# Performance work log

Hardware: AMD Instinct MI355X
Metric: run time of the kernel (lower is better)

Reference implementation:

```python
import jax, jax.numpy as jnp
import numpy as np

J0 = 3
JBIG = 7
TH = 0.01
MM = 3.2 ** 2  # Gaussian window variance factor from get_phi


def get_phi(x):
    # phi(x) = sinc-like sin(pi x)/(pi x) * exp(-x^2/(2*mm)), with phi(0)=1
    t = jnp.pi * x
    t_safe = jnp.where(t == 0.0, 1.0, t)
    out = jnp.sin(t) * jnp.exp(-jnp.square(x) / (2.0 * MM)) / t_safe
    return jnp.where(t == 0.0, 1.0, out)


def nearest_idx(x, targets):
    # x: [N,1], targets: [K] -> index of nearest sample for each target, [K]
    return jnp.argmin(jnp.abs(x - targets[None, :]), axis=0)


def _outer_recon(wc, wr, C):
    # sum_{c,r} wc[:,c] wr[:,r] C[c,r]  (equivalent to the blockwise einsum +
    # tensordot over flattened (c,r) pairs in the torch code)
    return jnp.einsum('nc,cr,mr->nm', wc, C, wr)


def setup_inputs() -> dict:
    key = jax.random.key(0)
    k_img, k_xc, k_xr = jax.random.split(key, 3)
    N = 4096
    img = jax.random.normal(k_img, (N, N), dtype=jnp.float32)
    # sorted sample coordinates in [-1, 1] (domain spanned by wavelet translates)
    xc = jnp.sort(2.0 * jax.random.uniform(k_xc, (N, 1), dtype=jnp.float32) - 1.0, axis=0)
    xr = jnp.sort(2.0 * jax.random.uniform(k_xr, (N, 1), dtype=jnp.float32) - 1.0, axis=0)
    return {"img": img, "xc": xc, "xr": xr}


def reference(img, xc, xr):
    # ---- coarse approximation at scale j0 ----
    j0 = J0
    k = jnp.asarray(np.arange(-2 ** j0, 2 ** j0 + 1, 1), dtype=jnp.float32)  # [K0]
    phi_c = get_phi((2.0 ** j0) * xc - k[None, :])  # [N, K0]
    phi_r = get_phi((2.0 ** j0) * xr - k[None, :])  # [N, K0]
    xjk = k * (2.0 ** (-j0))
    ic = nearest_idx(xc, xjk)
    ir = nearest_idx(xr, xjk)
    F = img[ic[:, None], ir[None, :]]               # [K0, K0]
    approx = _outer_recon(phi_c, phi_r, F)          # [N, N]

    # ---- detail scales j0 .. J-1 ----
    for j in range(J0, JBIG):
        kj = jnp.asarray(np.arange((-2 ** (j + 1) - 1) / 2, 2 ** (j + 1) / 2, 0.5),
                         dtype=jnp.float32)          # [Kj] = 2^{j+2}+1
        xjk = (2.0 * kj + 1.0) * (2.0 ** (-j - 1))
        ic = nearest_idx(xc, xjk)
        ir = nearest_idx(xr, xjk)
        f = img[ic[:, None], ir[None, :]]            # [Kj, Kj]
        u = approx[ic[:, None], ir[None, :]]         # [Kj, Kj]
        diff = f - u
        # thresholded coefficient selection (torch.where -> mask, same math)
        D = jnp.where(jnp.abs(diff) > TH, diff, 0.0)
        psi_c = get_phi((2.0 ** (j + 1)) * xc - (2.0 * kj + 1.0)[None, :])  # [N, Kj]
        psi_r = get_phi((2.0 ** (j + 1)) * xr - (2.0 * kj + 1.0)[None, :])  # [N, Kj]
        approx = approx + _outer_recon(psi_c, psi_r, D)
    return approx
```

## Files before the change

### kernel.cpp

```cpp
#include <hip/hip_runtime.h>
#include <hip/hip_bf16.h>
#include <cstddef>
#include <cstdint>

#define NN 4096
#define KP 512
#define KTOT 501

typedef __attribute__((ext_vector_type(8))) short short8;
typedef __attribute__((ext_vector_type(4))) float f32x4;

#define GLB(p) ((const __attribute__((address_space(1))) void*)(p))
#define LDS(p) ((__attribute__((address_space(3))) void*)(p))

__device__ __forceinline__ float bf2f(unsigned short u) {
    union { unsigned int i; float f; } v; v.i = ((unsigned int)u) << 16; return v.f;
}

__device__ __forceinline__ void split_bf16(float v, unsigned short& h, unsigned short& l) {
    __hip_bfloat16 hb = __float2bfloat16(v);
    __hip_bfloat16 lb = __float2bfloat16(v - __bfloat162float(hb));
    h = *(unsigned short*)&hb;
    l = *(unsigned short*)&lb;
}

__device__ __forceinline__ float phi_eval(float x) {
    if (x == 0.0f) return 1.0f;
    const float PI_F = 3.14159265358979323846f;
    float rn = rintf(x);
    float r  = x - rn;
    float s  = __sinf(PI_F * r);
    if (((int)rn) & 1) s = -s;
    float e  = __expf(-x * x * (1.0f / 20.48f));
    return __fdividef(s * e, PI_F * x);
}

__device__ __forceinline__ void col_to_level(int col, int& l, int& off) {
    if      (col < 17)  { l = 0; off = 0;   }
    else if (col < 50)  { l = 1; off = 17;  }
    else if (col < 115) { l = 2; off = 50;  }
    else                { l = (col < 244) ? 3 : 4; off = (col < 244) ? 115 : 244; }
}

__global__ __launch_bounds__(256) void fused_pre(const float* __restrict__ xc,
                                                 const float* __restrict__ xr,
                                                 unsigned short* __restrict__ PCh,
                                                 unsigned short* __restrict__ PCl,
                                                 unsigned short* __restrict__ PRh,
                                                 unsigned short* __restrict__ PRl,
                                                 unsigned short* __restrict__ Ch,
                                                 int* __restrict__ idxAll) {
    __shared__ float sv[256];
    __shared__ int   si[256];
    const int b = blockIdx.x;
    const int tid = threadIdx.x;
    if (b < 2 * KTOT) {
        int side = (b >= KTOT);
        int col  = side ? b - KTOT : b;
        const float* x = side ? xr : xc;
        int l, off; col_to_level(col, l, off);
        int s = 8 << l;
        float target = (float)(col - off - s) / (float)s;
        float best = 1e30f; int bidx = 0;
        for (int n = tid; n < NN; n += 256) {
            float d = fabsf(x[n] - target);
            if (d < best) { best = d; bidx = n; }
        }
        sv[tid] = best; si[tid] = bidx;
        __syncthreads();
        for (int w = 128; w > 0; w >>= 1) {
            if (tid < w) {
                float ov = sv[tid + w]; int oi = si[tid + w];
                if (ov < sv[tid] || (ov == sv[tid] && oi < si[tid])) { sv[tid] = ov; si[tid] = oi; }
            }
            __syncthreads();
        }
        if (tid == 0) idxAll[b] = si[0];
    } else if (b < 2026) {
        const int i0 = (b - 1002) * 2048 + tid;
        #pragma unroll
        for (int j = 0; j < 8; ++j) {
            int i = i0 + j * 256;
            int n = i >> 9, col = i & 511;
            float pc = 0.f, pr = 0.f;
            if (col < KTOT) {
                int l, off; col_to_level(col, l, off);
                int s = 8 << l;
                float fo = (float)(col - off - s);
                float fs = (float)s;
                pc = phi_eval(fs * xc[n] - fo);
                pr = phi_eval(fs * xr[n] - fo);
            }
            unsigned short h, l2;
            split_bf16(pc, h, l2); PCh[i] = h; PCl[i] = l2;
            split_bf16(pr, h, l2); PRh[i] = h; PRl[i] = l2;
        }
    } else {
        uint4* z = (uint4*)Ch;
        const int g0 = (b - 2026) * 256 + tid;
        #pragma unroll
        for (int j = 0; j < 8; ++j) {
            int g = g0 + j * 8192;
            z[g] = make_uint4(0u, 0u, 0u, 0u);
        }
    }
}


template<int T, int OFF>
__global__ __launch_bounds__(256) void build_k(const float* __restrict__ img,
                                               const int* __restrict__ idxAll,
                                               const float* __restrict__ Usm,
                                               const unsigned short* __restrict__ PRh,
                                               const unsigned short* __restrict__ PRl,
                                               float* __restrict__ CdT,
                                               unsigned short* __restrict__ Ch,
                                               unsigned short* __restrict__ Cl) {
    int i = blockIdx.x * 256 + threadIdx.x;
    if (i >= T * T) return;
    int p = i / T, q = i - p * T;
    int ip = idxAll[OFF + p];
    int iq = idxAll[KTOT + OFF + q];
    float f = img[(size_t)ip * NN + iq];
    float val;
    if (OFF == 0) {
        val = f;
    } else {
        const float* u = Usm + (size_t)(OFF + p) * KP;
        const unsigned short* ph = PRh + (size_t)iq * KP;
        const unsigned short* pl = PRl + (size_t)iq * KP;
        float s0 = 0.f, s1 = 0.f, s2 = 0.f, s3 = 0.f;
        int k = 0;
        #pragma unroll 4
        for (; k + 4 <= OFF; k += 4) {
            ushort4 h4 = *(const ushort4*)(ph + k);
            ushort4 l4 = *(const ushort4*)(pl + k);
            float4  b4 = *(const float4*)(u + k);
            s0 += (bf2f(h4.x) + bf2f(l4.x)) * b4.x;
            s1 += (bf2f(h4.y) + bf2f(l4.y)) * b4.y;
            s2 += (bf2f(h4.z) + bf2f(l4.z)) * b4.z;
            s3 += (bf2f(h4.w) + bf2f(l4.w)) * b4.w;
        }
        float uu = (s0 + s1) + (s2 + s3);
        for (; k < OFF; ++k) uu += (bf2f(ph[k]) + bf2f(pl[k])) * u[k];
        float d = f - uu;
        val = (fabsf(d) > 0.01f) ? d : 0.0f;
    }
    size_t o = (size_t)(OFF + q) * KP + (OFF + p);
    CdT[o] = val;
    unsigned short h, l;
    split_bf16(val, h, l);
    Ch[o] = h; Cl[o] = l;
}

template<int T, int OFF>
__global__ __launch_bounds__(256) void update_k(const unsigned short* __restrict__ PCh,
                                                const unsigned short* __restrict__ PCl,
                                                const int* __restrict__ idxAll,
                                                const float* __restrict__ CdT,
                                                float* __restrict__ Usm) {
    int i = blockIdx.x * 256 + threadIdx.x;
    if (i >= KTOT * T) return;
    int r = i / T, t = i - r * T;
    const unsigned short* ah = PCh + (size_t)idxAll[r] * KP + OFF;
    const unsigned short* al = PCl + (size_t)idxAll[r] * KP + OFF;
    const float* b = CdT + (size_t)(OFF + t) * KP + OFF;
    constexpr int HEAD = (4 - (OFF & 3)) & 3;
    float s = 0.f;
    int k = 0;
    #pragma unroll
    for (; k < HEAD; ++k) s += (bf2f(ah[k]) + bf2f(al[k])) * b[k];
    float s0 = 0.f, s1 = 0.f, s2 = 0.f, s3 = 0.f;
    #pragma unroll 4
    for (; k + 4 <= T; k += 4) {
        ushort4 h4 = *(const ushort4*)(ah + k);
        ushort4 l4 = *(const ushort4*)(al + k);
        float4  b4 = *(const float4*)(b + k);
        s0 += (bf2f(h4.x) + bf2f(l4.x)) * b4.x;
        s1 += (bf2f(h4.y) + bf2f(l4.y)) * b4.y;
        s2 += (bf2f(h4.z) + bf2f(l4.z)) * b4.z;
        s3 += (bf2f(h4.w) + bf2f(l4.w)) * b4.w;
    }
    s += (s0 + s1) + (s2 + s3);
    for (; k < T; ++k) s += (bf2f(ah[k]) + bf2f(al[k])) * b[k];
    Usm[(size_t)r * KP + OFF + t] = s;
}

#define GEMM_BODY(Ahi_, Alo_, Bhi_, Blo_, XARR_, XBASE_, BMASK_)                       \
    __shared__ short As_h[2][128][32];                                                 \
    __shared__ short As_l[2][128][32];                                                 \
    __shared__ short Bs_h[2][128][32];                                                 \
    __shared__ short Bs_l[2][128][32];                                                 \
    const int tid  = threadIdx.x;                                                      \
    const int lane = tid & 63;                                                         \
    const int wave = tid >> 6;                                                         \
    const int wr   = wave >> 1;                                                        \
    const int wc   = wave & 1;                                                         \
    const int row0 = blockIdx.y * 128;                                                 \
    const int col0 = blockIdx.x * 128;                                                 \
    int list[16]; int nch = 0;                                                         \
    {                                                                                  \
        float xmn = XARR_[XBASE_];                                                     \
        float xmx = XARR_[(XBASE_) + 127];                                             \
        int mask = 0;                                                                  \
        const int off_[5] = {0, 17, 50, 115, 244};                                     \
        _Pragma("unroll")                                                              \
        for (int l = 0; l < 5; ++l) {                                                  \
            int s_ = 8 << l;                                                           \
            int clo = off_[l] + s_ + (int)floorf(s_ * xmn - 12.5f);                    \
            int chi = off_[l] + s_ + (int)ceilf (s_ * xmx + 12.5f);                    \
            if (clo < off_[l]) clo = off_[l];                                          \
            if (chi > off_[l] + 2 * s_) chi = off_[l] + 2 * s_;                        \
            for (int c = clo >> 5; c <= (chi >> 5); ++c) mask |= 1 << c;               \
        }                                                                              \
        mask &= (BMASK_);                                                              \
        for (int c = 0; c < 16; ++c) if ((mask >> c) & 1) list[nch++] = c;             \
    }                                                                                  \
    f32x4 acc[4][4];                                                                   \
    _Pragma("unroll")                                                                  \
    for (int i = 0; i < 4; ++i)                                                        \
        _Pragma("unroll")                                                              \
        for (int j = 0; j < 4; ++j) acc[i][j] = (f32x4){0.f, 0.f, 0.f, 0.f};           \
    const int srow = lane >> 2;                                                        \
    const int scol = ((lane & 3) ^ ((lane >> 3) & 3)) * 8;    \
    auto stage_ = [&](int bb, int k0) {                                                \
        _Pragma("unroll")                                                              \
        for (int s = 0; s < 2; ++s) {                                                  \
            const int rseg = wave * 32 + s * 16;                                       \
            const size_t ga = (size_t)(row0 + rseg + srow) * KP + k0 + scol;           \
            const size_t gb = (size_t)(col0 + rseg + srow) * KP + k0 + scol;           \
            __builtin_amdgcn_global_load_lds(GLB(Ahi_ + ga), LDS(&As_h[bb][rseg][0]), 16, 0, 0); \
            __builtin_amdgcn_global_load_lds(GLB(Alo_ + ga), LDS(&As_l[bb][rseg][0]), 16, 0, 0); \
            __builtin_amdgcn_global_load_lds(GLB(Bhi_ + gb), LDS(&Bs_h[bb][rseg][0]), 16, 0, 0); \
            __builtin_amdgcn_global_load_lds(GLB(Blo_ + gb), LDS(&Bs_l[bb][rseg][0]), 16, 0, 0); \
        }                                                                              \
    };                                                                                 \
    const int kbsw = 8 * ((lane >> 4) ^ ((lane >> 1) & 3));    \
    if (nch > 0) stage_(0, list[0] * 32);                                              \
    __syncthreads();                                                                   \
    for (int ic = 0; ic < nch; ++ic) {                                                 \
        const int cb = ic & 1;                                                         \
        if (ic + 1 < nch) stage_(cb ^ 1, list[ic + 1] * 32);                           \
        short8 ah[4], al[4], bh[4], bl[4];                                             \
        _Pragma("unroll")                                                              \
        for (int mb = 0; mb < 4; ++mb) {                                               \
            const int rr = wr * 64 + mb * 16 + (lane & 15);                            \
            ah[mb] = *(const short8*)&As_h[cb][rr][kbsw];                              \
            al[mb] = *(const short8*)&As_l[cb][rr][kbsw];                              \
        }                                                                              \
        _Pragma("unroll")                                                              \
        for (int nb = 0; nb < 4; ++nb) {                                               \
            const int cc = wc * 64 + nb * 16 + (lane & 15);                            \
            bh[nb] = *(const short8*)&Bs_h[cb][cc][kbsw];                              \
            bl[nb] = *(const short8*)&Bs_l[cb][cc][kbsw];                              \
        }                                                                              \
        _Pragma("unroll")                                                              \
        for (int mb = 0; mb < 4; ++mb)                                                 \
            _Pragma("unroll")                                                          \
            for (int nb = 0; nb < 4; ++nb) {                                           \
                acc[mb][nb] = __builtin_amdgcn_mfma_f32_16x16x32_bf16(ah[mb], bh[nb], acc[mb][nb], 0, 0, 0); \
                acc[mb][nb] = __builtin_amdgcn_mfma_f32_16x16x32_bf16(ah[mb], bl[nb], acc[mb][nb], 0, 0, 0); \
                acc[mb][nb] = __builtin_amdgcn_mfma_f32_16x16x32_bf16(al[mb], bh[nb], acc[mb][nb], 0, 0, 0); \
            }                                                                          \
        __syncthreads();                                                               \
    }                                                                                  \
    const int orow = (lane >> 4) * 4;                                                  \
    const int ocol = lane & 15;

__global__ __launch_bounds__(256) void gemm_mfma_f32out(const short* __restrict__ Ahi,
                                                        const short* __restrict__ Alo,
                                                        const short* __restrict__ Bhi,
                                                        const short* __restrict__ Blo,
                                                        const float* __restrict__ xr,
                                                        float* __restrict__ out) {
    GEMM_BODY(Ahi, Alo, Bhi, Blo, xr, blockIdx.x * 128, 0xFFFF)
    #pragma unroll
    for (int mb = 0; mb < 4; ++mb)
        #pragma unroll
        for (int nb = 0; nb < 4; ++nb) {
            const int col = col0 + wc * 64 + nb * 16 + ocol;
            #pragma unroll
            for (int reg = 0; reg < 4; ++reg) {
                const int row = row0 + wr * 64 + mb * 16 + orow + reg;
                out[(size_t)row * NN + col] = acc[mb][nb][reg];
            }
        }
}

__global__ __launch_bounds__(256) void gemm_mfma_splitout(const short* __restrict__ Ahi,
                                                          const short* __restrict__ Alo,
                                                          const short* __restrict__ Bhi,
                                                          const short* __restrict__ Blo,
                                                          const float* __restrict__ xc,
                                                          unsigned short* __restrict__ Oh,
                                                          unsigned short* __restrict__ Ol) {
    const int bmask_tab[4] = {0x00FF, 0xFFF8, 0xFF80, 0xFF80};
    const int bm = bmask_tab[blockIdx.x];
    GEMM_BODY(Ahi, Alo, Bhi, Blo, xc, blockIdx.y * 128, bm)
    #pragma unroll
    for (int mb = 0; mb < 4; ++mb)
        #pragma unroll
        for (int nb = 0; nb < 4; ++nb) {
            const int col = col0 + wc * 64 + nb * 16 + ocol;
            #pragma unroll
            for (int reg = 0; reg < 4; ++reg) {
                const int row = row0 + wr * 64 + mb * 16 + orow + reg;
                unsigned short h, l;
                split_bf16(acc[mb][nb][reg], h, l);
                Oh[(size_t)row * KP + col] = h;
                Ol[(size_t)row * KP + col] = l;
            }
        }
}

extern "C" void kernel_launch(void* const* d_in, const int* in_sizes, int n_in,
                              void* d_out, int out_size, void* d_ws, size_t ws_size,
                              hipStream_t stream) {
    const float* img = (const float*)d_in[0];
    const float* xc  = (const float*)d_in[1];
    const float* xr  = (const float*)d_in[2];
    float* out = (float*)d_out;

    const size_t M2 = (size_t)NN * KP;
    unsigned short* PCh = (unsigned short*)d_ws;
    unsigned short* PCl = PCh + M2;
    unsigned short* PRh = PCl + M2;
    unsigned short* PRl = PRh + M2;
    unsigned short* Uh  = PRl + M2;
    unsigned short* Ul  = Uh + M2;
    float* Usm = (float*)(Ul + M2);
    float* CdT = Usm + (size_t)KP * KP;
    unsigned short* Ch = (unsigned short*)(CdT + (size_t)KP * KP);
    unsigned short* Cl = Ch + (size_t)KP * KP;
    int* idxAll = (int*)(Cl + (size_t)KP * KP);

    fused_pre<<<dim3(2058), 256, 0, stream>>>(xc, xr, PCh, PCl, PRh, PRl, Ch, idxAll);
    build_k<17, 0>   <<<dim3(2),   256, 0, stream>>>(img, idxAll, Usm, PRh, PRl, CdT, Ch, Cl);
    update_k<17, 0>  <<<dim3(34),  256, 0, stream>>>(PCh, PCl, idxAll, CdT, Usm);
    build_k<33, 17>  <<<dim3(5),   256, 0, stream>>>(img, idxAll, Usm, PRh, PRl, CdT, Ch, Cl);
    update_k<33, 17> <<<dim3(65),  256, 0, stream>>>(PCh, PCl, idxAll, CdT, Usm);
    build_k<65, 50>  <<<dim3(17),  256, 0, stream>>>(img, idxAll, Usm, PRh, PRl, CdT, Ch, Cl);
    update_k<65, 50> <<<dim3(128), 256, 0, stream>>>(PCh, PCl, idxAll, CdT, Usm);
    build_k<129, 115><<<dim3(66),  256, 0, stream>>>(img, idxAll, Usm, PRh, PRl, CdT, Ch, Cl);
    update_k<129, 115><<<dim3(253), 256, 0, stream>>>(PCh, PCl, idxAll, CdT, Usm);
    build_k<257, 244><<<dim3(259), 256, 0, stream>>>(img, idxAll, Usm, PRh, PRl, CdT, Ch, Cl);
    gemm_mfma_splitout<<<dim3(KP / 128, NN / 128), 256, 0, stream>>>(
        (const short*)PCh, (const short*)PCl, (const short*)Ch, (const short*)Cl, xc, Uh, Ul);
    gemm_mfma_f32out<<<dim3(NN / 128, NN / 128), 256, 0, stream>>>(
        (const short*)Uh, (const short*)Ul, (const short*)PRh, (const short*)PRl, xr, out);
}
```

Baseline: 226.8 us.

## Fuse serial build/update chain into one cooperative kernel with grid syncs

Replaces the nine small build and update kernel launches with a single cooperative kernel of 256 blocks that runs each stage in a grid-stride loop, separated by grid-wide barriers. The aim is to remove per-launch overhead and the idle gaps between many tiny dependent kernels. In exchange, the template parameters become runtime values, which loses compile-time unrolling and constant division. The largest stage (257x257 with a long dot product) now runs on 256 blocks instead of 259, and each grid barrier adds its own cost.

Result: slower. 431.5 us (+90.2%).

```diff
diff --git a/kernel.cpp b/kernel.cpp
--- a/kernel.cpp
+++ b/kernel.cpp
@@ -1,7 +1,10 @@
 #include <hip/hip_runtime.h>
 #include <hip/hip_bf16.h>
+#include <hip/hip_cooperative_groups.h>
 #include <cstddef>
 #include <cstdint>
+
+namespace cg = cooperative_groups;
 
 #define NN 4096
 #define KP 512
@@ -107,83 +110,119 @@
 }
 
 
-template<int T, int OFF>
-__global__ __launch_bounds__(256) void build_k(const float* __restrict__ img,
-                                               const int* __restrict__ idxAll,
-                                               const float* __restrict__ Usm,
-                                               const unsigned short* __restrict__ PRh,
-                                               const unsigned short* __restrict__ PRl,
-                                               float* __restrict__ CdT,
-                                               unsigned short* __restrict__ Ch,
-                                               unsigned short* __restrict__ Cl) {
-    int i = blockIdx.x * 256 + threadIdx.x;
-    if (i >= T * T) return;
-    int p = i / T, q = i - p * T;
-    int ip = idxAll[OFF + p];
-    int iq = idxAll[KTOT + OFF + q];
-    float f = img[(size_t)ip * NN + iq];
-    float val;
-    if (OFF == 0) {
-        val = f;
-    } else {
-        const float* u = Usm + (size_t)(OFF + p) * KP;
-        const unsigned short* ph = PRh + (size_t)iq * KP;
-        const unsigned short* pl = PRl + (size_t)iq * KP;
+__device__ __forceinline__ void do_build(int T, int OFF,
+                                         const float* __restrict__ img,
+                                         const int* __restrict__ idxAll,
+                                         const float* __restrict__ Usm,
+                                         const unsigned short* __restrict__ PRh,
+                                         const unsigned short* __restrict__ PRl,
+                                         float* __restrict__ CdT,
+                                         unsigned short* __restrict__ Ch,
+                                         unsigned short* __restrict__ Cl,
+                                         int gid, int gsize) {
+    const int tot = T * T;
+    for (int i = gid; i < tot; i += gsize) {
+        int p = i / T, q = i - p * T;
+        int ip = idxAll[OFF + p];
+        int iq = idxAll[KTOT + OFF + q];
+        float f = img[(size_t)ip * NN + iq];
+        float val;
+        if (OFF == 0) {
+            val = f;
+        } else {
+            const float* u = Usm + (size_t)(OFF + p) * KP;
+            const unsigned short* ph = PRh + (size_t)iq * KP;
+            const unsigned short* pl = PRl + (size_t)iq * KP;
+            float s0 = 0.f, s1 = 0.f, s2 = 0.f, s3 = 0.f;
+            int k = 0;
+            #pragma unroll 4
+            for (; k + 4 <= OFF; k += 4) {
+                ushort4 h4 = *(const ushort4*)(ph + k);
+                ushort4 l4 = *(const ushort4*)(pl + k);
+                float4  b4 = *(const float4*)(u + k);
+                s0 += (bf2f(h4.x) + bf2f(l4.x)) * b4.x;
+                s1 += (bf2f(h4.y) + bf2f(l4.y)) * b4.y;
+                s2 += (bf2f(h4.z) + bf2f(l4.z)) * b4.z;
+                s3 += (bf2f(h4.w) + bf2f(l4.w)) * b4.w;
+            }
+            float uu = (s0 + s1) + (s2 + s3);
+            for (; k < OFF; ++k) uu += (bf2f(ph[k]) + bf2f(pl[k])) * u[k];
+            float d = f - uu;
+            val = (fabsf(d) > 0.01f) ? d : 0.0f;
+        }
+        size_t o = (size_t)(OFF + q) * KP + (OFF + p);
+        CdT[o] = val;
+        unsigned short h, l;
+        split_bf16(val, h, l);
+        Ch[o] = h; Cl[o] = l;
+    }
+}
+
+__device__ __forceinline__ void do_update(int T, int OFF,
+                                          const unsigned short* __restrict__ PCh,
+                                          const unsigned short* __restrict__ PCl,
+                                          const int* __restrict__ idxAll,
+                                          const float* __restrict__ CdT,
+                                          float* __restrict__ Usm,
+                                          int gid, int gsize) {
+    const int tot = KTOT * T;
+    const int HEAD = (4 - (OFF & 3)) & 3;
+    for (int i = gid; i < tot; i += gsize) {
+        int r = i / T, t = i - r * T;
+        const unsigned short* ah = PCh + (size_t)idxAll[r] * KP + OFF;
+        const unsigned short* al = PCl + (size_t)idxAll[r] * KP + OFF;
+        const float* b = CdT + (size_t)(OFF + t) * KP + OFF;
+        float s = 0.f;
+        int k = 0;
+        for (; k < HEAD; ++k) s += (bf2f(ah[k]) + bf2f(al[k])) * b[k];
         float s0 = 0.f, s1 = 0.f, s2 = 0.f, s3 = 0.f;
-        int k = 0;
         #pragma unroll 4
-        for (; k + 4 <= OFF; k += 4) {
-            ushort4 h4 = *(const ushort4*)(ph + k);
-            ushort4 l4 = *(const ushort4*)(pl + k);
-            float4  b4 = *(const float4*)(u + k);
+        for (; k + 4 <= T; k += 4) {
+            ushort4 h4 = *(const ushort4*)(ah + k);
+            ushort4 l4 = *(const ushort4*)(al + k);
+            float4  b4 = *(const float4*)(b + k);
             s0 += (bf2f(h4.x) + bf2f(l4.x)) * b4.x;
             s1 += (bf2f(h4.y) + bf2f(l4.y)) * b4.y;
             s2 += (bf2f(h4.z) + bf2f(l4.z)) * b4.z;
             s3 += (bf2f(h4.w) + bf2f(l4.w)) * b4.w;
         }
-        float uu = (s0 + s1) + (s2 + s3);
-        for (; k < OFF; ++k) uu += (bf2f(ph[k]) + bf2f(pl[k])) * u[k];
-        float d = f - uu;
-        val = (fabsf(d) > 0.01f) ? d : 0.0f;
+        s += (s0 + s1) + (s2 + s3);
+        for (; k < T; ++k) s += (bf2f(ah[k]) + bf2f(al[k])) * b[k];
+        Usm[(size_t)r * KP + OFF + t] = s;
     }
-    size_t o = (size_t)(OFF + q) * KP + (OFF + p);
-    CdT[o] = val;
-    unsigned short h, l;
-    split_bf16(val, h, l);
-    Ch[o] = h; Cl[o] = l;
-}
-
-template<int T, int OFF>
-__global__ __launch_bounds__(256) void update_k(const unsigned short* __restrict__ PCh,
-                                                const unsigned short* __restrict__ PCl,
-                                                const int* __restrict__ idxAll,
-                                                const float* __restrict__ CdT,
-                                                float* __restrict__ Usm) {
-    int i = blockIdx.x * 256 + threadIdx.x;
-    if (i >= KTOT * T) return;
-    int r = i / T, t = i - r * T;
-    const unsigned short* ah = PCh + (size_t)idxAll[r] * KP + OFF;
-    const unsigned short* al = PCl + (size_t)idxAll[r] * KP + OFF;
-    const float* b = CdT + (size_t)(OFF + t) * KP + OFF;
-    constexpr int HEAD = (4 - (OFF & 3)) & 3;
-    float s = 0.f;
-    int k = 0;
-    #pragma unroll
-    for (; k < HEAD; ++k) s += (bf2f(ah[k]) + bf2f(al[k])) * b[k];
-    float s0 = 0.f, s1 = 0.f, s2 = 0.f, s3 = 0.f;
-    #pragma unroll 4
-    for (; k + 4 <= T; k += 4) {
-        ushort4 h4 = *(const ushort4*)(ah + k);
-        ushort4 l4 = *(const ushort4*)(al + k);
-        float4  b4 = *(const float4*)(b + k);
-        s0 += (bf2f(h4.x) + bf2f(l4.x)) * b4.x;
-        s1 += (bf2f(h4.y) + bf2f(l4.y)) * b4.y;
-        s2 += (bf2f(h4.z) + bf2f(l4.z)) * b4.z;
-        s3 += (bf2f(h4.w) + bf2f(l4.w)) * b4.w;
-    }
-    s += (s0 + s1) + (s2 + s3);
-    for (; k < T; ++k) s += (bf2f(ah[k]) + bf2f(al[k])) * b[k];
-    Usm[(size_t)r * KP + OFF + t] = s;
+}
+
+__global__ __launch_bounds__(256) void chain_fused(const float* __restrict__ img,
+                                                   const int* __restrict__ idxAll,
+                                                   float* __restrict__ Usm,
+                                                   const unsigned short* __restrict__ PRh,
+                                                   const unsigned short* __restrict__ PRl,
+                                                   float* __restrict__ CdT,
+                                                   unsigned short* __restrict__ Ch,
+                                                   unsigned short* __restrict__ Cl,
+                                                   const unsigned short* __restrict__ PCh,
+                                                   const unsigned short* __restrict__ PCl) {
+    cg::grid_group grid = cg::this_grid();
+    const int gsize = gridDim.x * 256;
+    const int gid   = blockIdx.x * 256 + threadIdx.x;
+
+    do_build(17, 0, img, idxAll, Usm, PRh, PRl, CdT, Ch, Cl, gid, gsize);
+    grid.sync();
+    do_update(17, 0, PCh, PCl, idxAll, CdT, Usm, gid, gsize);
+    grid.sync();
+    do_build(33, 17, img, idxAll, Usm, PRh, PRl, CdT, Ch, Cl, gid, gsize);
+    grid.sync();
+    do_update(33, 17, PCh, PCl, idxAll, CdT, Usm, gid, gsize);
+    grid.sync();
+    do_build(65, 50, img, idxAll, Usm, PRh, PRl, CdT, Ch, Cl, gid, gsize);
+    grid.sync();
+    do_update(65, 50, PCh, PCl, idxAll, CdT, Usm, gid, gsize);
+    grid.sync();
+    do_build(129, 115, img, idxAll, Usm, PRh, PRl, CdT, Ch, Cl, gid, gsize);
+    grid.sync();
+    do_update(129, 115, PCh, PCl, idxAll, CdT, Usm, gid, gsize);
+    grid.sync();
+    do_build(257, 244, img, idxAll, Usm, PRh, PRl, CdT, Ch, Cl, gid, gsize);
 }
 
 #define GEMM_BODY(Ahi_, Alo_, Bhi_, Blo_, XARR_, XBASE_, BMASK_)                       \
@@ -335,15 +374,20 @@
     int* idxAll = (int*)(Cl + (size_t)KP * KP);
 
     fused_pre<<<dim3(2058), 256, 0, stream>>>(xc, xr, PCh, PCl, PRh, PRl, Ch, idxAll);
-    build_k<17, 0>   <<<dim3(2),   256, 0, stream>>>(img, idxAll, Usm, PRh, PRl, CdT, Ch, Cl);
-    update_k<17, 0>  <<<dim3(34),  256, 0, stream>>>(PCh, PCl, idxAll, CdT, Usm);
-    build_k<33, 17>  <<<dim3(5),   256, 0, stream>>>(img, idxAll, Usm, PRh, PRl, CdT, Ch, Cl);
-    update_k<33, 17> <<<dim3(65),  256, 0, stream>>>(PCh, PCl, idxAll, CdT, Usm);
-    build_k<65, 50>  <<<dim3(17),  256, 0, stream>>>(img, idxAll, Usm, PRh, PRl, CdT, Ch, Cl);
-    update_k<65, 50> <<<dim3(128), 256, 0, stream>>>(PCh, PCl, idxAll, CdT, Usm);
-    build_k<129, 115><<<dim3(66),  256, 0, stream>>>(img, idxAll, Usm, PRh, PRl, CdT, Ch, Cl);
-    update_k<129, 115><<<dim3(253), 256, 0, stream>>>(PCh, PCl, idxAll, CdT, Usm);
-    build_k<257, 244><<<dim3(259), 256, 0, stream>>>(img, idxAll, Usm, PRh, PRl, CdT, Ch, Cl);
+
+    {
+        const int* idxAllC = idxAll;
+        const unsigned short* PRhC = PRh;
+        const unsigned short* PRlC = PRl;
+        const unsigned short* PChC = PCh;
+        const unsigned short* PClC = PCl;
+        void* cargs[] = {(void*)&img, (void*)&idxAllC, (void*)&Usm,
+                         (void*)&PRhC, (void*)&PRlC, (void*)&CdT,
+                         (void*)&Ch, (void*)&Cl, (void*)&PChC, (void*)&PClC};
+        hipLaunchCooperativeKernel((const void*)chain_fused, dim3(256), dim3(256),
+                                   cargs, 0, stream);
+    }
+
     gemm_mfma_splitout<<<dim3(KP / 128, NN / 128), 256, 0, stream>>>(
         (const short*)PCh, (const short*)PCl, (const short*)Ch, (const short*)Cl, xc, Uh, Ul);
     gemm_mfma_f32out<<<dim3(NN / 128, NN / 128), 256, 0, stream>>>(
```

## Fuse per-scale coefficient build and Usm update into one kernel per level

Applied to the files above, without the earlier changes.

Merges each level's build_k and update_k pair into a single fold_k kernel. Each block owns one column t, computes the thresholded coefficients for that column into shared memory, then updates the Usm entries for the remaining rows with them. This removes four kernel launches and the CdT round trip through global memory. The cost is far fewer blocks per level (T blocks instead of hundreds), so parallelism is lower and each block loops serially over rows.

Result: faster. 220.6 us (-2.8%).

```diff
diff --git a/kernel.cpp b/kernel.cpp
--- a/kernel.cpp
+++ b/kernel.cpp
@@ -106,84 +106,118 @@
     }
 }
 
-
 template<int T, int OFF>
-__global__ __launch_bounds__(256) void build_k(const float* __restrict__ img,
-                                               const int* __restrict__ idxAll,
-                                               const float* __restrict__ Usm,
-                                               const unsigned short* __restrict__ PRh,
-                                               const unsigned short* __restrict__ PRl,
-                                               float* __restrict__ CdT,
-                                               unsigned short* __restrict__ Ch,
-                                               unsigned short* __restrict__ Cl) {
+__global__ __launch_bounds__(256) void fold_k(const float* __restrict__ img,
+                                              const int* __restrict__ idxAll,
+                                              float* __restrict__ Usm,
+                                              const unsigned short* __restrict__ PRh,
+                                              const unsigned short* __restrict__ PRl,
+                                              const unsigned short* __restrict__ PCh,
+                                              const unsigned short* __restrict__ PCl,
+                                              unsigned short* __restrict__ Ch,
+                                              unsigned short* __restrict__ Cl) {
+    __shared__ float vals[T];
+    const int t   = blockIdx.x;
+    const int tid = threadIdx.x;
+    const int iq  = idxAll[KTOT + OFF + t];
+
+    for (int p = tid; p < T; p += 256) {
+        int ip = idxAll[OFF + p];
+        float f = img[(size_t)ip * NN + iq];
+        float val;
+        if (OFF == 0) {
+            val = f;
+        } else {
+            const float* u = Usm + (size_t)(OFF + p) * KP;
+            const unsigned short* ph = PRh + (size_t)iq * KP;
+            const unsigned short* pl = PRl + (size_t)iq * KP;
+            float s0 = 0.f, s1 = 0.f, s2 = 0.f, s3 = 0.f;
+            int k = 0;
+            #pragma unroll 4
+            for (; k + 4 <= OFF; k += 4) {
+                ushort4 h4 = *(const ushort4*)(ph + k);
+                ushort4 l4 = *(const ushort4*)(pl + k);
+                float4  b4 = *(const float4*)(u + k);
+                s0 += (bf2f(h4.x) + bf2f(l4.x)) * b4.x;
+                s1 += (bf2f(h4.y) + bf2f(l4.y)) * b4.y;
+                s2 += (bf2f(h4.z) + bf2f(l4.z)) * b4.z;
+                s3 += (bf2f(h4.w) + bf2f(l4.w)) * b4.w;
+            }
+            float uu = (s0 + s1) + (s2 + s3);
+            for (; k < OFF; ++k) uu += (bf2f(ph[k]) + bf2f(pl[k])) * u[k];
+            float d = f - uu;
+            val = (fabsf(d) > 0.01f) ? d : 0.0f;
+        }
+        vals[p] = val;
+        size_t o = (size_t)(OFF + t) * KP + (OFF + p);
+        unsigned short h, l;
+        split_bf16(val, h, l);
+        Ch[o] = h; Cl[o] = l;
+    }
+    __syncthreads();
+
+    constexpr int R0 = OFF + T;
+    constexpr int HEAD = (4 - (OFF & 3)) & 3;
+    for (int r = R0 + tid; r < KTOT; r += 256) {
+        const unsigned short* ah = PCh + (size_t)idxAll[r] * KP + OFF;
+        const unsigned short* al = PCl + (size_t)idxAll[r] * KP + OFF;
+        float s = 0.f;
+        int k = 0;
+        #pragma unroll
+        for (; k < HEAD; ++k) s += (bf2f(ah[k]) + bf2f(al[k])) * vals[k];
+        float s0 = 0.f, s1 = 0.f, s2 = 0.f, s3 = 0.f;
+        #pragma unroll 4
+        for (; k + 4 <= T; k += 4) {
+            ushort4 h4 = *(const ushort4*)(ah + k);
+            ushort4 l4 = *(const ushort4*)(al + k);
+            s0 += (bf2f(h4.x) + bf2f(l4.x)) * vals[k];
+            s1 += (bf2f(h4.y) + bf2f(l4.y)) * vals[k + 1];
+            s2 += (bf2f(h4.z) + bf2f(l4.z)) * vals[k + 2];
+            s3 += (bf2f(h4.w) + bf2f(l4.w)) * vals[k + 3];
+        }
+        s += (s0 + s1) + (s2 + s3);
+        for (; k < T; ++k) s += (bf2f(ah[k]) + bf2f(al[k])) * vals[k];
+        Usm[(size_t)r * KP + OFF + t] = s;
+    }
+}
+
+__global__ __launch_bounds__(256) void build_last(const float* __restrict__ img,
+                                                  const int* __restrict__ idxAll,
+                                                  const float* __restrict__ Usm,
+                                                  const unsigned short* __restrict__ PRh,
+                                                  const unsigned short* __restrict__ PRl,
+                                                  unsigned short* __restrict__ Ch,
+                                                  unsigned short* __restrict__ Cl) {
+    constexpr int T = 257, OFF = 244;
     int i = blockIdx.x * 256 + threadIdx.x;
     if (i >= T * T) return;
     int p = i / T, q = i - p * T;
     int ip = idxAll[OFF + p];
     int iq = idxAll[KTOT + OFF + q];
     float f = img[(size_t)ip * NN + iq];
-    float val;
-    if (OFF == 0) {
-        val = f;
-    } else {
-        const float* u = Usm + (size_t)(OFF + p) * KP;
-        const unsigned short* ph = PRh + (size_t)iq * KP;
-        const unsigned short* pl = PRl + (size_t)iq * KP;
-        float s0 = 0.f, s1 = 0.f, s2 = 0.f, s3 = 0.f;
-        int k = 0;
-        #pragma unroll 4
-        for (; k + 4 <= OFF; k += 4) {
-            ushort4 h4 = *(const ushort4*)(ph + k);
-            ushort4 l4 = *(const ushort4*)(pl + k);
-            float4  b4 = *(const float4*)(u + k);
-            s0 += (bf2f(h4.x) + bf2f(l4.x)) * b4.x;
-            s1 += (bf2f(h4.y) + bf2f(l4.y)) * b4.y;
-            s2 += (bf2f(h4.z) + bf2f(l4.z)) * b4.z;
-            s3 += (bf2f(h4.w) + bf2f(l4.w)) * b4.w;
-        }
-        float uu = (s0 + s1) + (s2 + s3);
-        for (; k < OFF; ++k) uu += (bf2f(ph[k]) + bf2f(pl[k])) * u[k];
-        float d = f - uu;
-        val = (fabsf(d) > 0.01f) ? d : 0.0f;
-    }
-    size_t o = (size_t)(OFF + q) * KP + (OFF + p);
-    CdT[o] = val;
-    unsigned short h, l;
-    split_bf16(val, h, l);
-    Ch[o] = h; Cl[o] = l;
-}
-
-template<int T, int OFF>
-__global__ __launch_bounds__(256) void update_k(const unsigned short* __restrict__ PCh,
-                                                const unsigned short* __restrict__ PCl,
-                                                const int* __restrict__ idxAll,
-                                                const float* __restrict__ CdT,
-                                                float* __restrict__ Usm) {
-    int i = blockIdx.x * 256 + threadIdx.x;
-    if (i >= KTOT * T) return;
-    int r = i / T, t = i - r * T;
-    const unsigned short* ah = PCh + (size_t)idxAll[r] * KP + OFF;
-    const unsigned short* al = PCl + (size_t)idxAll[r] * KP + OFF;
-    const float* b = CdT + (size_t)(OFF + t) * KP + OFF;
-    constexpr int HEAD = (4 - (OFF & 3)) & 3;
-    float s = 0.f;
+    const float* u = Usm + (size_t)(OFF + p) * KP;
+    const unsigned short* ph = PRh + (size_t)iq * KP;
+    const unsigned short* pl = PRl + (size_t)iq * KP;
+    float s0 = 0.f, s1 = 0.f, s2 = 0.f, s3 = 0.f;
     int k = 0;
-    #pragma unroll
-    for (; k < HEAD; ++k) s += (bf2f(ah[k]) + bf2f(al[k])) * b[k];
-    float s0 = 0.f, s1 = 0.f, s2 = 0.f, s3 = 0.f;
     #pragma unroll 4
-    for (; k + 4 <= T; k += 4) {
-        ushort4 h4 = *(const ushort4*)(ah + k);
-        ushort4 l4 = *(const ushort4*)(al + k);
-        float4  b4 = *(const float4*)(b + k);
+    for (; k + 4 <= OFF; k += 4) {
+        ushort4 h4 = *(const ushort4*)(ph + k);
+        ushort4 l4 = *(const ushort4*)(pl + k);
+        float4  b4 = *(const float4*)(u + k);
         s0 += (bf2f(h4.x) + bf2f(l4.x)) * b4.x;
         s1 += (bf2f(h4.y) + bf2f(l4.y)) * b4.y;
         s2 += (bf2f(h4.z) + bf2f(l4.z)) * b4.z;
         s3 += (bf2f(h4.w) + bf2f(l4.w)) * b4.w;
     }
-    s += (s0 + s1) + (s2 + s3);
-    for (; k < T; ++k) s += (bf2f(ah[k]) + bf2f(al[k])) * b[k];
-    Usm[(size_t)r * KP + OFF + t] = s;
+    float uu = (s0 + s1) + (s2 + s3);
+    for (; k < OFF; ++k) uu += (bf2f(ph[k]) + bf2f(pl[k])) * u[k];
+    float d = f - uu;
+    float val = (fabsf(d) > 0.01f) ? d : 0.0f;
+    size_t o = (size_t)(OFF + q) * KP + (OFF + p);
+    unsigned short h, l;
+    split_bf16(val, h, l);
+    Ch[o] = h; Cl[o] = l;
 }
 
 #define GEMM_BODY(Ahi_, Alo_, Bhi_, Blo_, XARR_, XBASE_, BMASK_)                       \
@@ -335,15 +369,13 @@
     int* idxAll = (int*)(Cl + (size_t)KP * KP);
 
     fused_pre<<<dim3(2058), 256, 0, stream>>>(xc, xr, PCh, PCl, PRh, PRl, Ch, idxAll);
-    build_k<17, 0>   <<<dim3(2),   256, 0, stream>>>(img, idxAll, Usm, PRh, PRl, CdT, Ch, Cl);
-    update_k<17, 0>  <<<dim3(34),  256, 0, stream>>>(PCh, PCl, idxAll, CdT, Usm);
-    build_k<33, 17>  <<<dim3(5),   256, 0, stream>>>(img, idxAll, Usm, PRh, PRl, CdT, Ch, Cl);
-    update_k<33, 17> <<<dim3(65),  256, 0, stream>>>(PCh, PCl, idxAll, CdT, Usm);
-    build_k<65, 50>  <<<dim3(17),  256, 0, stream>>>(img, idxAll, Usm, PRh, PRl, CdT, Ch, Cl);
-    update_k<65, 50> <<<dim3(128), 256, 0, stream>>>(PCh, PCl, idxAll, CdT, Usm);
-    build_k<129, 115><<<dim3(66),  256, 0, stream>>>(img, idxAll, Usm, PRh, PRl, CdT, Ch, Cl);
-    update_k<129, 115><<<dim3(253), 256, 0, stream>>>(PCh, PCl, idxAll, CdT, Usm);
-    build_k<257, 244><<<dim3(259), 256, 0, stream>>>(img, idxAll, Usm, PRh, PRl, CdT, Ch, Cl);
+
+    fold_k<17, 0>   <<<dim3(17),  256, 0, stream>>>(img, idxAll, Usm, PRh, PRl, PCh, PCl, Ch, Cl);
+    fold_k<33, 17>  <<<dim3(33),  256, 0, stream>>>(img, idxAll, Usm, PRh, PRl, PCh, PCl, Ch, Cl);
+    fold_k<65, 50>  <<<dim3(65),  256, 0, stream>>>(img, idxAll, Usm, PRh, PRl, PCh, PCl, Ch, Cl);
+    fold_k<129, 115><<<dim3(129), 256, 0, stream>>>(img, idxAll, Usm, PRh, PRl, PCh, PCl, Ch, Cl);
+    build_last      <<<dim3(259), 256, 0, stream>>>(img, idxAll, Usm, PRh, PRl, Ch, Cl);
+
     gemm_mfma_splitout<<<dim3(KP / 128, NN / 128), 256, 0, stream>>>(
         (const short*)PCh, (const short*)PCl, (const short*)Ch, (const short*)Cl, xc, Uh, Ul);
     gemm_mfma_f32out<<<dim3(NN / 128, NN / 128), 256, 0, stream>>>(
```
